# Kernel tuning notes

Hardware: AMD Instinct MI355X
Metric: run time of the kernel (lower is better)

The kernel has to match this reference:

```python
import jax, jax.numpy as jnp
import numpy as np

B, C, H, W = 4, 128, 256, 256
HIDDEN = max(C // 8, 4)  # SE hidden


def haar_dwt(x):
    # x: (B,C,H,W), H,W even. Haar 2x2 stride-2 depthwise conv via block reshape.
    b_, c_, h_, w_ = x.shape
    xb = x.reshape(b_, c_, h_ // 2, 2, w_ // 2, 2)
    a = xb[:, :, :, 0, :, 0]
    b = xb[:, :, :, 0, :, 1]
    c = xb[:, :, :, 1, :, 0]
    d = xb[:, :, :, 1, :, 1]
    LL = 0.5 * (a + b + c + d)
    LH = 0.5 * (-a + b - c + d)
    HL = 0.5 * (-a - b + c + d)
    HH = 0.5 * (a - b - c + d)
    return LH, HL, HH, LL


def haar_idwt(LH, HL, HH, LL):
    # inverse of the depthwise conv_transpose with the same Haar kernels
    a = 0.5 * (LL - LH - HL + HH)
    b = 0.5 * (LL + LH - HL - HH)
    c = 0.5 * (LL - LH + HL - HH)
    d = 0.5 * (LL + LH + HL + HH)
    top = jnp.stack([a, b], axis=-1)      # (B,C,h,w,2)
    bot = jnp.stack([c, d], axis=-1)      # (B,C,h,w,2)
    blk = jnp.stack([top, bot], axis=-2)  # (B,C,h,w,2,2) -> rows x cols
    Bs, Cs, h, w = LL.shape
    return blk.transpose(0, 1, 2, 4, 3, 5).reshape(Bs, Cs, 2 * h, 2 * w)


def soft_threshold(x, thr):
    return jnp.sign(x) * jax.nn.relu(jnp.abs(x) - thr)


def setup_inputs() -> dict:
    key = jax.random.key(0)
    ks = jax.random.split(key, 9)
    x = jax.random.normal(ks[0], (B, C, H, W), dtype=jnp.float32)
    theta = jax.random.normal(ks[1], (3, C, 1, 1), dtype=jnp.float32) * 0.02
    dir_gate = jax.random.normal(ks[2], (3, C, 1, 1), dtype=jnp.float32) * 0.02
    fc_w = jax.random.normal(ks[3], (C, C), dtype=jnp.float32) * (1.0 / np.sqrt(C))
    fc_b = jax.random.normal(ks[4], (C,), dtype=jnp.float32) * 0.02
    sub_redistribute = jax.random.normal(ks[5], (C, 3), dtype=jnp.float32) * 0.02
    se_w1 = jax.random.normal(ks[6], (HIDDEN, C), dtype=jnp.float32) * (1.0 / np.sqrt(C))
    se_b1 = jnp.zeros((HIDDEN,), dtype=jnp.float32)
    se_w2 = jax.random.normal(ks[7], (C, HIDDEN), dtype=jnp.float32) * (1.0 / np.sqrt(HIDDEN))
    se_b2 = jnp.zeros((C,), dtype=jnp.float32)
    gamma = jnp.float32(0.5)
    return {"x": x, "theta": theta, "dir_gate": dir_gate, "fc_w": fc_w,
            "fc_b": fc_b, "sub_redistribute": sub_redistribute,
            "se_w1": se_w1, "se_b1": se_b1, "se_w2": se_w2, "se_b2": se_b2,
            "gamma": gamma}


def reference(x, theta, dir_gate, fc_w, fc_b, sub_redistribute,
              se_w1, se_b1, se_w2, se_b2, gamma):
    eps = 1e-6
    LH, HL, HH, LL = haar_dwt(x)

    # per-(B,C) abs-mean thresholds
    m_LH = jnp.mean(jnp.abs(LH), axis=(2, 3), keepdims=True) + eps
    m_HL = jnp.mean(jnp.abs(HL), axis=(2, 3), keepdims=True) + eps
    m_HH = jnp.mean(jnp.abs(HH), axis=(2, 3), keepdims=True) + eps
    t = jax.nn.sigmoid(theta)  # (3,C,1,1)
    LH_hat = soft_threshold(LH, t[0][None] * m_LH)
    HL_hat = soft_threshold(HL, t[1][None] * m_HL)
    HH_hat = soft_threshold(HH, t[2][None] * m_HH)

    g = jax.nn.sigmoid(dir_gate)
    LH_hat = LH_hat * g[0][None]
    HL_hat = HL_hat * g[1][None]
    HH_hat = HH_hat * g[2][None]

    stack3 = jnp.stack([LH_hat, HL_hat, HH_hat], axis=2)  # (B,C,3,h,w)
    attn_band = jax.nn.softmax(jnp.mean(jnp.abs(stack3), axis=1, keepdims=True), axis=2)
    H_mix = jnp.sum(stack3 * attn_band, axis=2)  # (B,C,h,w)

    w_redis = jax.nn.softmax(sub_redistribute, axis=1)  # (C,3)
    H_redist = H_mix[:, :, None] * w_redis[None, :, :, None, None]  # (B,C,3,h,w)
    X_re = haar_idwt(H_redist[:, :, 0], H_redist[:, :, 1], H_redist[:, :, 2], LL)

    # channel softmax gate from GAP + fc
    gap_vec = jnp.mean(X_re, axis=(2, 3))  # (B,C)
    gap_vec = gap_vec @ fc_w.T + fc_b
    w_softmax = jax.nn.softmax(gap_vec, axis=1)[:, :, None, None]

    # SE gate
    z = jnp.mean(X_re, axis=(2, 3))  # (B,C)
    z = jax.nn.relu(z @ se_w1.T + se_b1)
    w_se = jax.nn.sigmoid(z @ se_w2.T + se_b2)[:, :, None, None]

    return x * w_softmax + gamma * (X_re * w_se)
```

## Files before the change

### kernel.cpp

```cpp
#include <hip/hip_runtime.h>
#include <math.h>

#define BB 4
#define CC 128
#define WWW 256
#define HWSZ 65536
#define HIDDEN 16
#define NPAIR 8192
#define FCHUNK 16
#define NFCHUNK (NPAIR/FCHUNK)
#define RQUART 4

typedef float nfloat4 __attribute__((ext_vector_type(4)));

struct CParams {
    float thr0, thr1, thr2;
    float gA0, gA1, gA2;
    float gF0, gF1, gF2;
    float wsm, e0q;
    float ca, cb, cc, cd;
    float pad0;
};
static_assert(sizeof(CParams) == 64, "CParams must be 64B");

__device__ __forceinline__ float sigmoidf_(float v) { return 1.0f / (1.0f + expf(-v)); }

__global__ __launch_bounds__(256) void k_reduce(const float* __restrict__ x,
                                                float4* __restrict__ partial) {
    const int bq = blockIdx.x;
    const int bc = bq >> 2;
    const int quarter = bq & 3;
    const float* base = x + (size_t)bc * HWSZ;
    const int tid = threadIdx.x;
    float a0 = 0.f, a1 = 0.f, a2 = 0.f, sx = 0.f;
    #pragma unroll
    for (int i = 0; i < 8; ++i) {
        const int p = quarter * 2048 + i * 256 + tid;
        const int r = p >> 6;
        const int q = p & 63;
        const float4 t  = *(const float4*)(base + (2*r)   * WWW + 4*q);
        const float4 bo = *(const float4*)(base + (2*r+1) * WWW + 4*q);
        {   const float a = t.x, b_ = t.y, c_ = bo.x, d = bo.y;
            const float u1 = a + b_, u2 = c_ + d, u3 = a + c_, u4 = b_ + d, u5 = a + d, u6 = b_ + c_;
            a0 += fabsf(u4 - u3);
            a1 += fabsf(u2 - u1);
            a2 += fabsf(u5 - u6);
            sx += u1 + u2;
        }
        {   const float a = t.z, b_ = t.w, c_ = bo.z, d = bo.w;
            const float u1 = a + b_, u2 = c_ + d, u3 = a + c_, u4 = b_ + d, u5 = a + d, u6 = b_ + c_;
            a0 += fabsf(u4 - u3);
            a1 += fabsf(u2 - u1);
            a2 += fabsf(u5 - u6);
            sx += u1 + u2;
        }
    }
    __shared__ float4 red[256];
    red[tid] = make_float4(a0, a1, a2, sx);
    __syncthreads();
    for (int off = 128; off > 0; off >>= 1) {
        if (tid < off) {
            float4 o = red[tid + off];
            red[tid].x += o.x; red[tid].y += o.y; red[tid].z += o.z; red[tid].w += o.w;
        }
        __syncthreads();
    }
    if (tid == 0) partial[bq] = red[0];
}

__global__ __launch_bounds__(256) void k_fused(const float* __restrict__ x,
                                               const float4* __restrict__ partial,
    const float* __restrict__ theta, const float* __restrict__ dir_gate,
    const float* __restrict__ fc_w, const float* __restrict__ fc_b,
    const float* __restrict__ sub_r,
    const float* __restrict__ se_w1, const float* __restrict__ se_b1,
    const float* __restrict__ se_w2, const float* __restrict__ se_b2,
    const float* __restrict__ gamma_p,
    float* __restrict__ out) {
    const int b = blockIdx.y;
    const int chunk = blockIdx.x;
    const int tid = threadIdx.x;
    const int pp = tid & 15;
    const int g  = tid >> 4;

    __shared__ CParams cp[CC];
    __shared__ float red2[16][16][6];
    __shared__ float att2[16][4];
    __shared__ float gap[CC];
    __shared__ float z1[HIDDEN];
    __shared__ float yv[CC];
    __shared__ float ev[CC];

    float4 s = make_float4(0.f, 0.f, 0.f, 0.f);
    if (tid < CC) {
        #pragma unroll
        for (int k = 0; k < RQUART; ++k) {
            const float4 pq = partial[(b * CC + tid) * RQUART + k];
            s.x += pq.x; s.y += pq.y; s.z += pq.z; s.w += pq.w;
        }
        gap[tid] = s.w * (1.0f / 65536.0f);
    }
    __syncthreads();
    float y = 0.f;
    if (tid < CC) {
        y = fc_b[tid];
        for (int j = 0; j < CC; ++j) y += gap[j] * fc_w[tid * CC + j];
        yv[tid] = y;
    }
    if (tid < HIDDEN) {
        float z = se_b1[tid];
        for (int j = 0; j < CC; ++j) z += gap[j] * se_w1[tid * CC + j];
        z1[tid] = fmaxf(z, 0.0f);
    }
    __syncthreads();
    float e = 0.f;
    if (tid < CC) {
        float mx = -1e30f;
        for (int j = 0; j < CC; ++j) mx = fmaxf(mx, yv[j]);
        e = expf(y - mx);
        ev[tid] = e;
    }
    __syncthreads();
    if (tid < CC) {
        float ssum = 0.f;
        for (int j = 0; j < CC; ++j) ssum += ev[j];
        const float wsm = e / ssum;

        float wse = se_b2[tid];
        for (int h = 0; h < HIDDEN; ++h) wse += z1[h] * se_w2[tid * HIDDEN + h];
        wse = sigmoidf_(wse);
        const float wse2 = gamma_p[0] * wse;

        const float m0 = s.x * (0.5f / 16384.0f) + 1e-6f;
        const float m1 = s.y * (0.5f / 16384.0f) + 1e-6f;
        const float m2 = s.z * (0.5f / 16384.0f) + 1e-6f;
        CParams p;
        const float g0 = sigmoidf_(dir_gate[0 * CC + tid]);
        const float g1 = sigmoidf_(dir_gate[1 * CC + tid]);
        const float g2 = sigmoidf_(dir_gate[2 * CC + tid]);
        p.thr0 = 2.0f * sigmoidf_(theta[0 * CC + tid]) * m0;
        p.thr1 = 2.0f * sigmoidf_(theta[1 * CC + tid]) * m1;
        p.thr2 = 2.0f * sigmoidf_(theta[2 * CC + tid]) * m2;
        p.gA0 = g0; p.gA1 = g1; p.gA2 = g2;
        p.gF0 = 0.5f * g0 * wse2;
        p.gF1 = 0.5f * g1 * wse2;
        p.gF2 = 0.5f * g2 * wse2;
        p.wsm = wsm;
        p.e0q = 0.25f * wse2;
        const float r0 = sub_r[tid * 3 + 0], r1 = sub_r[tid * 3 + 1], r2 = sub_r[tid * 3 + 2];
        const float rm = fmaxf(r0, fmaxf(r1, r2));
        const float e0 = expf(r0 - rm), e1 = expf(r1 - rm), e2 = expf(r2 - rm);
        const float inv = 1.0f / (e0 + e1 + e2);
        const float w0 = e0 * inv, w1 = e1 * inv, w2 = e2 * inv;
        p.ca = 0.5f * (-w0 - w1 + w2);
        p.cb = 0.5f * ( w0 - w1 - w2);
        p.cc = 0.5f * (-w0 + w1 - w2);
        p.cd = 0.5f * ( w0 + w1 + w2);
        p.pad0 = 0.f;
        cp[tid] = p;
    }
    __syncthreads();

    const int p  = chunk * FCHUNK + pp;
    const int rp = p >> 6, q = p & 63;
    const float* base = x + (size_t)b * CC * HWSZ + (2*rp) * WWW + 4*q;

    float4 st[8], sb[8];
    float sA0=0, sA1=0, sA2=0, sB0=0, sB1=0, sB2=0;
    #pragma unroll
    for (int ci = 0; ci < 8; ++ci) {
        const int c = g * 8 + ci;
        const float* pc = base + c * HWSZ;
        st[ci] = *(const float4*)(pc);
        sb[ci] = *(const float4*)(pc + WWW);
        const float thr0 = cp[c].thr0, thr1 = cp[c].thr1, thr2 = cp[c].thr2;
        const float gA0 = cp[c].gA0, gA1 = cp[c].gA1, gA2 = cp[c].gA2;
        {   const float a = st[ci].x, b_ = st[ci].y, c_ = sb[ci].x, d = sb[ci].y;
            const float u1 = a + b_, u2 = c_ + d, u3 = a + c_, u4 = b_ + d, u5 = a + d, u6 = b_ + c_;
            sA0 += gA0 * fmaxf(fabsf(u4 - u3) - thr0, 0.f);
            sA1 += gA1 * fmaxf(fabsf(u2 - u1) - thr1, 0.f);
            sA2 += gA2 * fmaxf(fabsf(u5 - u6) - thr2, 0.f);
        }
        {   const float a = st[ci].z, b_ = st[ci].w, c_ = sb[ci].z, d = sb[ci].w;
            const float u1 = a + b_, u2 = c_ + d, u3 = a + c_, u4 = b_ + d, u5 = a + d, u6 = b_ + c_;
            sB0 += gA0 * fmaxf(fabsf(u4 - u3) - thr0, 0.f);
            sB1 += gA1 * fmaxf(fabsf(u2 - u1) - thr1, 0.f);
            sB2 += gA2 * fmaxf(fabsf(u5 - u6) - thr2, 0.f);
        }
    }
    red2[g][pp][0] = sA0; red2[g][pp][1] = sA1; red2[g][pp][2] = sA2;
    red2[g][pp][3] = sB0; red2[g][pp][4] = sB1; red2[g][pp][5] = sB2;
    __syncthreads();

    if (tid < 32) {
        const int pair = tid >> 1, h = tid & 1;
        float v0 = 0.f, v1 = 0.f, v2 = 0.f;
        #pragma unroll
        for (int gg = 0; gg < 16; ++gg) {
            v0 += red2[gg][pair][3*h + 0];
            v1 += red2[gg][pair][3*h + 1];
            v2 += red2[gg][pair][3*h + 2];
        }
        v0 *= (0.5f / CC); v1 *= (0.5f / CC); v2 *= (0.5f / CC);
        const float mx = fmaxf(v0, fmaxf(v1, v2));
        const float e0 = expf(v0 - mx), e1 = expf(v1 - mx), e2 = expf(v2 - mx);
        const float inv = 1.0f / (e0 + e1 + e2);
        att2[pair][2*h + 0] = e0 * inv;
        att2[pair][2*h + 1] = e1 * inv;
    }
    __syncthreads();

    const float a0A = att2[pp][0], a1A = att2[pp][1], a2A = 1.0f - a0A - a1A;
    const float a0B = att2[pp][2], a1B = att2[pp][3], a2B = 1.0f - a0B - a1B;

    float* obase = out + (size_t)b * CC * HWSZ + (2*rp) * WWW + 4*q;
    #pragma unroll
    for (int ci = 0; ci < 8; ++ci) {
        const int c = g * 8 + ci;
        const float thr0 = cp[c].thr0, thr1 = cp[c].thr1, thr2 = cp[c].thr2;
        const float gF0 = cp[c].gF0, gF1 = cp[c].gF1, gF2 = cp[c].gF2;
        const float wsm = cp[c].wsm, e0q = cp[c].e0q;
        const float ca = cp[c].ca, cb = cp[c].cb, ccc = cp[c].cc, cd = cp[c].cd;
        const float m0A = a0A * gF0, m1A = a1A * gF1, m2A = a2A * gF2;
        const float m0B = a0B * gF0, m1B = a1B * gF1, m2B = a2B * gF2;
        nfloat4 otop, obot;
        {   const float a = st[ci].x, b_ = st[ci].y, c_ = sb[ci].x, d = sb[ci].y;
            const float u1 = a + b_, u2 = c_ + d, u3 = a + c_, u4 = b_ + d, u5 = a + d, u6 = b_ + c_;
            const float B0 = u4 - u3, B1 = u2 - u1, B2 = u5 - u6;
            const float LL2 = u1 + u2;
            const float s0 = copysignf(fmaxf(fabsf(B0) - thr0, 0.f), B0);
            const float s1 = copysignf(fmaxf(fabsf(B1) - thr1, 0.f), B1);
            const float s2 = copysignf(fmaxf(fabsf(B2) - thr2, 0.f), B2);
            const float Hf = s0*m0A + s1*m1A + s2*m2A;
            const float T  = e0q * LL2;
            otop.x = fmaf(a , wsm, fmaf(Hf, ca , T));
            otop.y = fmaf(b_, wsm, fmaf(Hf, cb , T));
            obot.x = fmaf(c_, wsm, fmaf(Hf, ccc, T));
            obot.y = fmaf(d , wsm, fmaf(Hf, cd , T));
        }
        {   const float a = st[ci].z, b_ = st[ci].w, c_ = sb[ci].z, d = sb[ci].w;
            const float u1 = a + b_, u2 = c_ + d, u3 = a + c_, u4 = b_ + d, u5 = a + d, u6 = b_ + c_;
            const float B0 = u4 - u3, B1 = u2 - u1, B2 = u5 - u6;
            const float LL2 = u1 + u2;
            const float s0 = copysignf(fmaxf(fabsf(B0) - thr0, 0.f), B0);
            const float s1 = copysignf(fmaxf(fabsf(B1) - thr1, 0.f), B1);
            const float s2 = copysignf(fmaxf(fabsf(B2) - thr2, 0.f), B2);
            const float Hf = s0*m0B + s1*m1B + s2*m2B;
            const float T  = e0q * LL2;
            otop.z = fmaf(a , wsm, fmaf(Hf, ca , T));
            otop.w = fmaf(b_, wsm, fmaf(Hf, cb , T));
            obot.z = fmaf(c_, wsm, fmaf(Hf, ccc, T));
            obot.w = fmaf(d , wsm, fmaf(Hf, cd , T));
        }
        float* po = obase + c * HWSZ;
        __builtin_nontemporal_store(otop, (nfloat4*)(po));
        __builtin_nontemporal_store(obot, (nfloat4*)(po + WWW));
    }
}

extern "C" void kernel_launch(void* const* d_in, const int* in_sizes, int n_in,
                              void* d_out, int out_size, void* d_ws, size_t ws_size,
                              hipStream_t stream) {
    const float* x        = (const float*)d_in[0];
    const float* theta    = (const float*)d_in[1];
    const float* dir_gate = (const float*)d_in[2];
    const float* fc_w     = (const float*)d_in[3];
    const float* fc_b     = (const float*)d_in[4];
    const float* sub_r    = (const float*)d_in[5];
    const float* se_w1    = (const float*)d_in[6];
    const float* se_b1    = (const float*)d_in[7];
    const float* se_w2    = (const float*)d_in[8];
    const float* se_b2    = (const float*)d_in[9];
    const float* gamma_p  = (const float*)d_in[10];
    float* out = (float*)d_out;

    float4* partial = (float4*)d_ws;

    k_reduce<<<dim3(BB * CC * RQUART), dim3(256), 0, stream>>>(x, partial);
    k_fused<<<dim3(NFCHUNK, BB), dim3(256), 0, stream>>>(x, partial,
                                                theta, dir_gate, fc_w, fc_b,
                                                sub_r, se_w1, se_b1, se_w2, se_b2,
                                                gamma_p, out);
}
```

Baseline: 90.26 us.

## Compute per-channel gate params once per batch in last reduce block

Before, every one of the 2048 k_fused blocks recomputed the GAP, FC matvec, softmax, SE MLP and per-channel thresholds redundantly. Now the last k_reduce block for each batch, found with an atomic counter and threadfence, does this once and writes CParams to a workspace buffer. k_fused then just copies 8KB of parameters into shared memory. The cost is a memset launch, atomics, and a serialized tail in the reduce kernel.

Result: slower. 147.7 us (+63.6%).

```diff
diff --git a/kernel.cpp b/kernel.cpp
--- a/kernel.cpp
+++ b/kernel.cpp
@@ -10,6 +10,7 @@
 #define FCHUNK 16
 #define NFCHUNK (NPAIR/FCHUNK)
 #define RQUART 4
+#define RBLK_PER_B (CC*RQUART)
 
 typedef float nfloat4 __attribute__((ext_vector_type(4)));
 
@@ -26,10 +27,19 @@
 __device__ __forceinline__ float sigmoidf_(float v) { return 1.0f / (1.0f + expf(-v)); }
 
 __global__ __launch_bounds__(256) void k_reduce(const float* __restrict__ x,
-                                                float4* __restrict__ partial) {
+                                                float4* __restrict__ partial,
+                                                unsigned int* __restrict__ counters,
+    const float* __restrict__ theta, const float* __restrict__ dir_gate,
+    const float* __restrict__ fc_w, const float* __restrict__ fc_b,
+    const float* __restrict__ sub_r,
+    const float* __restrict__ se_w1, const float* __restrict__ se_b1,
+    const float* __restrict__ se_w2, const float* __restrict__ se_b2,
+    const float* __restrict__ gamma_p,
+    CParams* __restrict__ cbuf) {
     const int bq = blockIdx.x;
     const int bc = bq >> 2;
     const int quarter = bq & 3;
+    const int b = bq >> 9;
     const float* base = x + (size_t)bc * HWSZ;
     const int tid = threadIdx.x;
     float a0 = 0.f, a1 = 0.f, a2 = 0.f, sx = 0.f;
@@ -65,32 +75,20 @@
         }
         __syncthreads();
     }
-    if (tid == 0) partial[bq] = red[0];
-}
-
-__global__ __launch_bounds__(256) void k_fused(const float* __restrict__ x,
-                                               const float4* __restrict__ partial,
-    const float* __restrict__ theta, const float* __restrict__ dir_gate,
-    const float* __restrict__ fc_w, const float* __restrict__ fc_b,
-    const float* __restrict__ sub_r,
-    const float* __restrict__ se_w1, const float* __restrict__ se_b1,
-    const float* __restrict__ se_w2, const float* __restrict__ se_b2,
-    const float* __restrict__ gamma_p,
-    float* __restrict__ out) {
-    const int b = blockIdx.y;
-    const int chunk = blockIdx.x;
-    const int tid = threadIdx.x;
-    const int pp = tid & 15;
-    const int g  = tid >> 4;
-
-    __shared__ CParams cp[CC];
-    __shared__ float red2[16][16][6];
-    __shared__ float att2[16][4];
+    __shared__ int is_last;
+    if (tid == 0) {
+        partial[bq] = red[0];
+        __threadfence();
+        const unsigned int old = atomicAdd(&counters[b], 1u);
+        is_last = (old == RBLK_PER_B - 1) ? 1 : 0;
+    }
+    __syncthreads();
+    if (!is_last) return;
+    __threadfence();
+
     __shared__ float gap[CC];
     __shared__ float z1[HIDDEN];
     __shared__ float yv[CC];
-    __shared__ float ev[CC];
-
     float4 s = make_float4(0.f, 0.f, 0.f, 0.f);
     if (tid < CC) {
         #pragma unroll
@@ -113,6 +111,7 @@
         z1[tid] = fmaxf(z, 0.0f);
     }
     __syncthreads();
+    __shared__ float ev[CC];
     float e = 0.f;
     if (tid < CC) {
         float mx = -1e30f;
@@ -157,7 +156,26 @@
         p.cc = 0.5f * (-w0 + w1 - w2);
         p.cd = 0.5f * ( w0 + w1 + w2);
         p.pad0 = 0.f;
-        cp[tid] = p;
+        cbuf[b * CC + tid] = p;
+    }
+}
+
+__global__ __launch_bounds__(256) void k_fused(const float* __restrict__ x,
+                                               const CParams* __restrict__ cbuf,
+                                               float* __restrict__ out) {
+    const int b = blockIdx.y;
+    const int chunk = blockIdx.x;
+    const int tid = threadIdx.x;
+    const int pp = tid & 15;
+    const int g  = tid >> 4;
+
+    __shared__ CParams cp[CC];
+    __shared__ float red2[16][16][6];
+    __shared__ float att2[16][4];
+    {
+        const float* src = (const float*)(cbuf + b * CC);
+        float* dst = (float*)cp;
+        for (int i = tid; i < CC * 16; i += 256) dst[i] = src[i];
     }
     __syncthreads();
 
@@ -274,11 +292,14 @@
     const float* gamma_p  = (const float*)d_in[10];
     float* out = (float*)d_out;
 
-    float4* partial = (float4*)d_ws;
-
-    k_reduce<<<dim3(BB * CC * RQUART), dim3(256), 0, stream>>>(x, partial);
-    k_fused<<<dim3(NFCHUNK, BB), dim3(256), 0, stream>>>(x, partial,
-                                                theta, dir_gate, fc_w, fc_b,
-                                                sub_r, se_w1, se_b1, se_w2, se_b2,
-                                                gamma_p, out);
+    char* ws = (char*)d_ws;
+    float4*       partial  = (float4*)(ws);
+    CParams*      cbuf     = (CParams*)(ws + 32768);
+    unsigned int* counters = (unsigned int*)(ws + 65536);
+
+    hipMemsetAsync(counters, 0, BB * sizeof(unsigned int), stream);
+    k_reduce<<<dim3(BB * CC * RQUART), dim3(256), 0, stream>>>(
+        x, partial, counters, theta, dir_gate, fc_w, fc_b,
+        sub_r, se_w1, se_b1, se_w2, se_b2, gamma_p, cbuf);
+    k_fused<<<dim3(NFCHUNK, BB), dim3(256), 0, stream>>>(x, cbuf, out);
 }
```
